# Kernel optimization log

Measured on AMD Instinct MI355X. Metric: run time of the kernel, lower is better.

## Reference

```python
import jax, jax.numpy as jnp
import numpy as np

N = 50000      # nodes
E = 800000     # edges (before self loops)
IN = 256       # in_channels
HID = 64       # hidden_channels
HEADS = 2
NEG_SLOPE = 0.2
BN_EPS = 1e-5


def setup_inputs() -> dict:
    key = jax.random.key(0)
    ks = jax.random.split(key, 16)
    def g(i, shape, scale=0.05):
        return jax.random.normal(ks[i], shape, dtype=jnp.float32) * scale
    return {
        "x": jax.random.normal(ks[0], (N, IN), dtype=jnp.float32),
        "edge_index": jax.random.randint(ks[1], (2, E), 0, N, dtype=jnp.int64).astype(jnp.int32),
        # conv1 (GATv2, heads=2, concat)
        "W1l": g(2, (IN, HEADS * HID)), "b1l": jnp.zeros(HEADS * HID, jnp.float32),
        "W1r": g(3, (IN, HEADS * HID)), "b1r": jnp.zeros(HEADS * HID, jnp.float32),
        "att1": g(4, (HEADS, HID)), "bias1": jnp.zeros(HEADS * HID, jnp.float32),
        "bn1_g": jnp.ones(HEADS * HID, jnp.float32), "bn1_b": jnp.zeros(HEADS * HID, jnp.float32),
        "bn1_m": jnp.zeros(HEADS * HID, jnp.float32), "bn1_v": jnp.ones(HEADS * HID, jnp.float32),
        # conv2 (GATv2, heads=1)
        "W2l": g(5, (HEADS * HID, HID)), "b2l": jnp.zeros(HID, jnp.float32),
        "W2r": g(6, (HEADS * HID, HID)), "b2r": jnp.zeros(HID, jnp.float32),
        "att2": g(7, (1, HID)), "bias2": jnp.zeros(HID, jnp.float32),
        "bn2_g": jnp.ones(HID, jnp.float32), "bn2_b": jnp.zeros(HID, jnp.float32),
        "bn2_m": jnp.zeros(HID, jnp.float32), "bn2_v": jnp.ones(HID, jnp.float32),
        # classifier
        "Wc": g(8, (HID, 1)), "bc": jnp.zeros(1, jnp.float32),
    }


def _gatv2(x, src, dst, Wl, bl, Wr, br, att, bias, heads, ch, n):
    # GATv2: e_ij = att . leaky_relu(Wl x_j + Wr x_i); segment softmax over dst; out_i = sum alpha_ij Wl x_j
    xl = (x @ Wl + bl).reshape(n, heads, ch)  # source transform [N,H,C]
    xr = (x @ Wr + br).reshape(n, heads, ch)  # target transform [N,H,C]
    e = jax.nn.leaky_relu(xl[src] + xr[dst], NEG_SLOPE)        # [E,H,C]
    logits = jnp.einsum('ehc,hc->eh', e, att)                  # [E,H]
    m = jax.ops.segment_max(logits, dst, num_segments=n)       # [N,H]
    p = jnp.exp(logits - m[dst])
    s = jax.ops.segment_sum(p, dst, num_segments=n)            # [N,H]
    alpha = p / s[dst]                                         # [E,H]
    out = jax.ops.segment_sum(alpha[:, :, None] * xl[src], dst, num_segments=n)  # [N,H,C]
    return out.reshape(n, heads * ch) + bias


def _bn(x, g, b, m, v):
    return (x - m) * jax.lax.rsqrt(v + BN_EPS) * g + b


def reference(x, edge_index, W1l, b1l, W1r, b1r, att1, bias1,
              bn1_g, bn1_b, bn1_m, bn1_v,
              W2l, b2l, W2r, b2r, att2, bias2,
              bn2_g, bn2_b, bn2_m, bn2_v, Wc, bc):
    n = x.shape[0]
    loop = jnp.arange(n, dtype=edge_index.dtype)  # add_self_loops=True
    src = jnp.concatenate([edge_index[0], loop])
    dst = jnp.concatenate([edge_index[1], loop])
    h = _gatv2(x, src, dst, W1l, b1l, W1r, b1r, att1, bias1, HEADS, HID, n)
    h = jax.nn.elu(_bn(h, bn1_g, bn1_b, bn1_m, bn1_v))
    h = _gatv2(h, src, dst, W2l, b2l, W2r, b2r, att2, bias2, 1, HID, n)
    h = jax.nn.elu(_bn(h, bn2_g, bn2_b, bn2_m, bn2_v))
    return jax.nn.sigmoid(h @ Wc + bc)
```

## Files before the change

### kernel.cpp

```cpp
#include <hip/hip_runtime.h>
#include <hip/hip_bf16.h>
#include <cstddef>

#define NN 50000
#define EE 800000
#define TE 850000
#define INC 256
#define C1 128
#define C2 64
#define NCHUNK 49

#define NB_COUNT 3321
#define NB_CAST  12500
#define NB_P1    256
#define NB_P2    128
#define NB_K1    (NB_COUNT + NB_CAST + NB_P1 + NB_P2)
#define NB_GEMM1 782
#define NB_K2    (NB_GEMM1 + NB_COUNT)

typedef unsigned short ushort_t;
typedef short bf16x8 __attribute__((ext_vector_type(8)));
typedef float f32x4 __attribute__((ext_vector_type(4)));

__device__ inline ushort_t bf16r(float f) {
    unsigned u = __float_as_uint(f);
    unsigned r = (u + 0x7fffu + ((u >> 16) & 1u)) >> 16;
    return (ushort_t)r;
}
#define LOF(u) (__uint_as_float((u) << 16))
#define HIF(u) (__uint_as_float((u) & 0xffff0000u))
#define LRELU(t) (fmaxf((t), 0.f) + 0.2f * fminf((t), 0.f))
#define ELU(t) ((t) > 0.f ? (t) : (__expf(t) - 1.f))


__global__ void k_scan1(const int* __restrict__ deg, int* __restrict__ incl,
                        int* __restrict__ totals) {
    __shared__ int lds[1024];
    int t = threadIdx.x;
    int i = blockIdx.x * 1024 + t;
    int v = (i < NN) ? deg[i] : 0;
    lds[t] = v;
    __syncthreads();
    for (int off = 1; off < 1024; off <<= 1) {
        int add = (t >= off) ? lds[t - off] : 0;
        __syncthreads();
        lds[t] += add;
        __syncthreads();
    }
    if (i < NN) incl[i] = lds[t];
    if (t == 1023) totals[blockIdx.x] = lds[t];
}

__global__ void k_scan2(const int* __restrict__ totals, int* __restrict__ chunkoff) {
    int t = threadIdx.x;
    int orig = (t < NCHUNK) ? totals[t] : 0;
    int v = orig;
    for (int off = 1; off < 64; off <<= 1) {
        int u = __shfl_up(v, off, 64);
        if (t >= off) v += u;
    }
    if (t < NCHUNK) chunkoff[t] = v - orig;
}

__global__ void k_scan3(const int* __restrict__ incl, const int* __restrict__ deg,
                        const int* __restrict__ chunkoff, int* __restrict__ rowstart) {
    int i = blockIdx.x * blockDim.x + threadIdx.x;
    if (i == 0) rowstart[NN] = TE;
    if (i >= NN) return;
    rowstart[i] = incl[i] - deg[i] + chunkoff[i >> 10];
}


__global__ __launch_bounds__(256) void k_stage1(
    const int* __restrict__ ei, int* __restrict__ deg, int* __restrict__ rank,
    const float* __restrict__ x, ushort_t* __restrict__ xb,
    const float* __restrict__ W1l, const float* __restrict__ W1r,
    const float* __restrict__ b1l, const float* __restrict__ b1r,
    ushort_t* __restrict__ Wt1, float* __restrict__ biasf1,
    const float* __restrict__ W2l, const float* __restrict__ W2r,
    const float* __restrict__ b2l, const float* __restrict__ b2r,
    ushort_t* __restrict__ Wt2, float* __restrict__ biasf2) {
    int b = blockIdx.x;
    int tid = threadIdx.x;
    if (b < NB_COUNT) {
        int e = b * 256 + tid;
        if (e < TE) {
            int dst = (e < EE) ? ei[EE + e] : (e - EE);
            rank[e] = atomicAdd(&deg[dst], 1);
        }
    } else if (b < NB_COUNT + NB_CAST) {
        int i = (b - NB_COUNT) * 256 + tid;
        float4 a = ((const float4*)x)[i];
        ushort4 o;
        o.x = bf16r(a.x); o.y = bf16r(a.y); o.z = bf16r(a.z); o.w = bf16r(a.w);
        ((ushort4*)xb)[i] = o;
    } else if (b < NB_COUNT + NB_CAST + NB_P1) {
        int n = b - NB_COUNT - NB_CAST;
        int k = tid;
        const float* W = (n < 128) ? W1l : W1r;
        int c = (n < 128) ? n : n - 128;
        Wt1[(size_t)n * 256 + k] = bf16r(W[(size_t)k * 128 + c]);
        if (n == 0) biasf1[k] = (k < 128) ? b1l[k] : b1r[k - 128];
    } else {
        int n = b - NB_COUNT - NB_CAST - NB_P1;
        int k = tid;
        if (k < 128) {
            const float* W = (n < 64) ? W2l : W2r;
            int c = (n < 64) ? n : n - 64;
            Wt2[(size_t)n * 128 + k] = bf16r(W[(size_t)k * 64 + c]);
            if (n == 0) biasf2[k] = (k < 64) ? b2l[k] : b2r[k - 64];
        }
    }
}


template <int K, int NCOL>
__device__ inline void gemm_body(const ushort_t* __restrict__ A,
                                 const ushort_t* __restrict__ Bt,
                                 const float* __restrict__ bias,
                                 ushort_t* __restrict__ C, int M,
                                 int bm, int bn, ushort_t* As, ushort_t* Bs) {
    int tid = threadIdx.x;
    int w = tid >> 6, l = tid & 63;
    int wm = (w & 1) * 64, wn = (w >> 1) * 64;
    int lm = l & 15, half = l >> 4;

    f32x4 zero = {0.f, 0.f, 0.f, 0.f};
    f32x4 acc[4][4];
#pragma unroll
    for (int a = 0; a < 4; a++)
#pragma unroll
        for (int b = 0; b < 4; b++) acc[a][b] = zero;

    for (int k0 = 0; k0 < K; k0 += 32) {
#pragma unroll
        for (int q = 0; q < 2; q++) {
            int seg = q * 256 + tid;
            int m = seg >> 2;
            int ko = (seg & 3) * 8;
            *(float4*)&As[m * 40 + ko] = *(const float4*)&A[(size_t)(bm + m) * K + k0 + ko];
            *(float4*)&Bs[m * 40 + ko] = *(const float4*)&Bt[(size_t)(bn + m) * K + k0 + ko];
        }
        __syncthreads();
        bf16x8 af[4], bfr[4];
#pragma unroll
        for (int mi = 0; mi < 4; mi++)
            af[mi] = *(const bf16x8*)&As[(wm + mi * 16 + lm) * 40 + half * 8];
#pragma unroll
        for (int ni = 0; ni < 4; ni++)
            bfr[ni] = *(const bf16x8*)&Bs[(wn + ni * 16 + lm) * 40 + half * 8];
#pragma unroll
        for (int mi = 0; mi < 4; mi++)
#pragma unroll
            for (int ni = 0; ni < 4; ni++)
                acc[mi][ni] = __builtin_amdgcn_mfma_f32_16x16x32_bf16(
                    af[mi], bfr[ni], acc[mi][ni], 0, 0, 0);
        __syncthreads();
    }
#pragma unroll
    for (int ni = 0; ni < 4; ni++) {
        int col = bn + wn + ni * 16 + lm;
        float bv = bias[col];
#pragma unroll
        for (int mi = 0; mi < 4; mi++) {
            int rbase = bm + wm + mi * 16 + half * 4;
#pragma unroll
            for (int r = 0; r < 4; r++) {
                int row = rbase + r;
                if (row < M) C[(size_t)row * NCOL + col] = bf16r(acc[mi][ni][r] + bv);
            }
        }
    }
}


__global__ __launch_bounds__(256) void k_gemm1_scatter(
    const ushort_t* __restrict__ A, const ushort_t* __restrict__ Bt,
    const float* __restrict__ bias, ushort_t* __restrict__ C,
    const int* __restrict__ ei, const int* __restrict__ rank,
    const int* __restrict__ rowstart, int* __restrict__ ssrc) {
    __shared__ __align__(16) ushort_t As[128 * 40];
    __shared__ __align__(16) ushort_t Bs[128 * 40];
    int b = blockIdx.x;
    if (b < NB_GEMM1) {
        int bm = (b >> 1) * 128;
        int bn = (b & 1) * 128;
        gemm_body<256, 256>(A, Bt, bias, C, NN, bm, bn, As, Bs);
    } else {
        int e = (b - NB_GEMM1) * 256 + threadIdx.x;
        if (e < TE) {
            int s, d;
            if (e < EE) { s = ei[e]; d = ei[EE + e]; }
            else        { s = e - EE; d = s; }
            ssrc[rowstart[d] + rank[e]] = s;
        }
    }
}

__global__ __launch_bounds__(256) void k_gemm2(
    const ushort_t* __restrict__ A, const ushort_t* __restrict__ Bt,
    const float* __restrict__ bias, ushort_t* __restrict__ C) {
    __shared__ __align__(16) ushort_t As[128 * 40];
    __shared__ __align__(16) ushort_t Bs[128 * 40];
    int bm = blockIdx.x * 128;
    gemm_body<128, 128>(A, Bt, bias, C, NN, bm, 0, As, Bs);
}


__global__ __launch_bounds__(256) void k_fused1(
    const ushort_t* __restrict__ xlr, const int* __restrict__ rowstart,
    const int* __restrict__ ssrc, const float* __restrict__ att,
    const float* __restrict__ bias,
    const float* __restrict__ g, const float* __restrict__ b,
    const float* __restrict__ m, const float* __restrict__ v,
    ushort_t* __restrict__ out) {
    int lane = threadIdx.x & 63;
    int i = blockIdx.x * 4 + (threadIdx.x >> 6);
    if (i >= NN) return;
    int hw = lane >> 5;
    int c2 = lane & 31;
    uint2 xru = *(const uint2*)&xlr[(size_t)i * 256 + 128 + 4 * c2];
    float xr0 = LOF(xru.x), xr1 = HIF(xru.x), xr2 = LOF(xru.y), xr3 = HIF(xru.y);
    float4 at = *(const float4*)&att[4 * c2];
    int row = rowstart[i], end = rowstart[i + 1];
    float a0 = 0.f, a1 = 0.f, a2 = 0.f, a3 = 0.f, s = 0.f;
    int j = row;
    for (; j + 8 <= end; j += 8) {
        int src[4];
        uint2 u[4];
#pragma unroll
        for (int k = 0; k < 4; k++) src[k] = ssrc[j + 2 * k + hw];
#pragma unroll
        for (int k = 0; k < 4; k++)
            u[k] = *(const uint2*)&xlr[(size_t)src[k] * 256 + 4 * c2];
        float d[4], f0[4], f1[4], f2[4], f3[4];
#pragma unroll
        for (int k = 0; k < 4; k++) {
            f0[k] = LOF(u[k].x); f1[k] = HIF(u[k].x);
            f2[k] = LOF(u[k].y); f3[k] = HIF(u[k].y);
            float t0 = f0[k] + xr0, t1 = f1[k] + xr1;
            float t2 = f2[k] + xr2, t3 = f3[k] + xr3;
            d[k] = at.x * LRELU(t0) + at.y * LRELU(t1)
                 + at.z * LRELU(t2) + at.w * LRELU(t3);
        }
#pragma unroll
        for (int o = 1; o <= 8; o <<= 1) {
#pragma unroll
            for (int k = 0; k < 4; k++) d[k] += __shfl_xor(d[k], o, 64);
        }
#pragma unroll
        for (int k = 0; k < 4; k++) {
            float p = __expf(d[k]);
            a0 += p * f0[k]; a1 += p * f1[k];
            a2 += p * f2[k]; a3 += p * f3[k];
            s += p;
        }
    }
    for (; j < end; j += 2) {
        int je = j + hw;
        bool valid = je < end;
        int src = valid ? ssrc[je] : i;
        uint2 uu = *(const uint2*)&xlr[(size_t)src * 256 + 4 * c2];
        float f0 = LOF(uu.x), f1 = HIF(uu.x), f2 = LOF(uu.y), f3 = HIF(uu.y);
        float t0 = f0 + xr0, t1 = f1 + xr1, t2 = f2 + xr2, t3 = f3 + xr3;
        float d = at.x * LRELU(t0) + at.y * LRELU(t1)
                + at.z * LRELU(t2) + at.w * LRELU(t3);
        d += __shfl_xor(d, 1, 64);
        d += __shfl_xor(d, 2, 64);
        d += __shfl_xor(d, 4, 64);
        d += __shfl_xor(d, 8, 64);
        float p = valid ? __expf(d) : 0.f;
        a0 += p * f0; a1 += p * f1; a2 += p * f2; a3 += p * f3;
        s += p;
    }
    a0 += __shfl_xor(a0, 32, 64);
    a1 += __shfl_xor(a1, 32, 64);
    a2 += __shfl_xor(a2, 32, 64);
    a3 += __shfl_xor(a3, 32, 64);
    s  += __shfl_xor(s, 32, 64);
    if (hw == 0) {
        float inv = 1.f / s;
        float4 bb = *(const float4*)&bias[4 * c2];
        float4 mm = *(const float4*)&m[4 * c2];
        float4 vv = *(const float4*)&v[4 * c2];
        float4 gg = *(const float4*)&g[4 * c2];
        float4 b2 = *(const float4*)&b[4 * c2];
        float o0 = a0 * inv + bb.x, o1 = a1 * inv + bb.y;
        float o2 = a2 * inv + bb.z, o3 = a3 * inv + bb.w;
        o0 = (o0 - mm.x) * rsqrtf(vv.x + 1e-5f) * gg.x + b2.x;
        o1 = (o1 - mm.y) * rsqrtf(vv.y + 1e-5f) * gg.y + b2.y;
        o2 = (o2 - mm.z) * rsqrtf(vv.z + 1e-5f) * gg.z + b2.z;
        o3 = (o3 - mm.w) * rsqrtf(vv.w + 1e-5f) * gg.w + b2.w;
        o0 = ELU(o0); o1 = ELU(o1); o2 = ELU(o2); o3 = ELU(o3);
        uint2 wp;
        wp.x = (unsigned)bf16r(o0) | ((unsigned)bf16r(o1) << 16);
        wp.y = (unsigned)bf16r(o2) | ((unsigned)bf16r(o3) << 16);
        *(uint2*)&out[(size_t)i * C1 + 4 * c2] = wp;
    }
}

__global__ __launch_bounds__(256) void k_fused2(
    const ushort_t* __restrict__ xlr, const int* __restrict__ rowstart,
    const int* __restrict__ ssrc, const float* __restrict__ att,
    const float* __restrict__ bias,
    const float* __restrict__ g, const float* __restrict__ b,
    const float* __restrict__ m, const float* __restrict__ v,
    const float* __restrict__ Wc, const float* __restrict__ bc,
    float* __restrict__ out) {
    int lane = threadIdx.x & 63;
    int i = blockIdx.x * 4 + (threadIdx.x >> 6);
    if (i >= NN) return;
    int qw = lane >> 4;
    int c4 = lane & 15;
    uint2 xru = *(const uint2*)&xlr[(size_t)i * 128 + 64 + 4 * c4];
    float xr0 = LOF(xru.x), xr1 = HIF(xru.x), xr2 = LOF(xru.y), xr3 = HIF(xru.y);
    float4 at = *(const float4*)&att[4 * c4];
    int row = rowstart[i], end = rowstart[i + 1];
    float a0 = 0.f, a1 = 0.f, a2 = 0.f, a3 = 0.f, s = 0.f;
    int j = row;
    for (; j + 8 <= end; j += 8) {
        int src[2];
        uint2 u[2];
#pragma unroll
        for (int k = 0; k < 2; k++) src[k] = ssrc[j + 4 * k + qw];
#pragma unroll
        for (int k = 0; k < 2; k++)
            u[k] = *(const uint2*)&xlr[(size_t)src[k] * 128 + 4 * c4];
        float d[2], f0[2], f1[2], f2[2], f3[2];
#pragma unroll
        for (int k = 0; k < 2; k++) {
            f0[k] = LOF(u[k].x); f1[k] = HIF(u[k].x);
            f2[k] = LOF(u[k].y); f3[k] = HIF(u[k].y);
            float t0 = f0[k] + xr0, t1 = f1[k] + xr1;
            float t2 = f2[k] + xr2, t3 = f3[k] + xr3;
            d[k] = at.x * LRELU(t0) + at.y * LRELU(t1)
                 + at.z * LRELU(t2) + at.w * LRELU(t3);
        }
#pragma unroll
        for (int o = 1; o <= 8; o <<= 1) {
#pragma unroll
            for (int k = 0; k < 2; k++) d[k] += __shfl_xor(d[k], o, 64);
        }
#pragma unroll
        for (int k = 0; k < 2; k++) {
            float p = __expf(d[k]);
            a0 += p * f0[k]; a1 += p * f1[k];
            a2 += p * f2[k]; a3 += p * f3[k];
            s += p;
        }
    }
    for (; j < end; j += 4) {
        int je = j + qw;
        bool valid = je < end;
        int src = valid ? ssrc[je] : i;
        uint2 uu = *(const uint2*)&xlr[(size_t)src * 128 + 4 * c4];
        float f0 = LOF(uu.x), f1 = HIF(uu.x), f2 = LOF(uu.y), f3 = HIF(uu.y);
        float t0 = f0 + xr0, t1 = f1 + xr1, t2 = f2 + xr2, t3 = f3 + xr3;
        float d = at.x * LRELU(t0) + at.y * LRELU(t1)
                + at.z * LRELU(t2) + at.w * LRELU(t3);
        d += __shfl_xor(d, 1, 64);
        d += __shfl_xor(d, 2, 64);
        d += __shfl_xor(d, 4, 64);
        d += __shfl_xor(d, 8, 64);
        float p = valid ? __expf(d) : 0.f;
        a0 += p * f0; a1 += p * f1; a2 += p * f2; a3 += p * f3;
        s += p;
    }
#pragma unroll
    for (int o = 16; o <= 32; o <<= 1) {
        a0 += __shfl_xor(a0, o, 64);
        a1 += __shfl_xor(a1, o, 64);
        a2 += __shfl_xor(a2, o, 64);
        a3 += __shfl_xor(a3, o, 64);
        s  += __shfl_xor(s, o, 64);
    }
    float inv = 1.f / s;
    float4 bb = *(const float4*)&bias[4 * c4];
    float4 mm = *(const float4*)&m[4 * c4];
    float4 vv = *(const float4*)&v[4 * c4];
    float4 gg = *(const float4*)&g[4 * c4];
    float4 b2 = *(const float4*)&b[4 * c4];
    float o0 = a0 * inv + bb.x, o1 = a1 * inv + bb.y;
    float o2 = a2 * inv + bb.z, o3 = a3 * inv + bb.w;
    o0 = (o0 - mm.x) * rsqrtf(vv.x + 1e-5f) * gg.x + b2.x;
    o1 = (o1 - mm.y) * rsqrtf(vv.y + 1e-5f) * gg.y + b2.y;
    o2 = (o2 - mm.z) * rsqrtf(vv.z + 1e-5f) * gg.z + b2.z;
    o3 = (o3 - mm.w) * rsqrtf(vv.w + 1e-5f) * gg.w + b2.w;
    o0 = ELU(o0); o1 = ELU(o1); o2 = ELU(o2); o3 = ELU(o3);
    float4 wc = *(const float4*)&Wc[4 * c4];
    float z = o0 * wc.x + o1 * wc.y + o2 * wc.z + o3 * wc.w;
    z += __shfl_xor(z, 1, 64);
    z += __shfl_xor(z, 2, 64);
    z += __shfl_xor(z, 4, 64);
    z += __shfl_xor(z, 8, 64);
    if (lane == 0) out[i] = 1.f / (1.f + __expf(-(z + bc[0])));
}


extern "C" void kernel_launch(void* const* d_in, const int* in_sizes, int n_in,
                              void* d_out, int out_size, void* d_ws, size_t ws_size,
                              hipStream_t stream) {
    const float* x    = (const float*)d_in[0];
    const int*   ei   = (const int*)d_in[1];
    const float* W1l  = (const float*)d_in[2];
    const float* b1l  = (const float*)d_in[3];
    const float* W1r  = (const float*)d_in[4];
    const float* b1r  = (const float*)d_in[5];
    const float* att1 = (const float*)d_in[6];
    const float* bias1= (const float*)d_in[7];
    const float* bn1g = (const float*)d_in[8];
    const float* bn1b = (const float*)d_in[9];
    const float* bn1m = (const float*)d_in[10];
    const float* bn1v = (const float*)d_in[11];
    const float* W2l  = (const float*)d_in[12];
    const float* b2l  = (const float*)d_in[13];
    const float* W2r  = (const float*)d_in[14];
    const float* b2r  = (const float*)d_in[15];
    const float* att2 = (const float*)d_in[16];
    const float* bias2= (const float*)d_in[17];
    const float* bn2g = (const float*)d_in[18];
    const float* bn2b = (const float*)d_in[19];
    const float* bn2m = (const float*)d_in[20];
    const float* bn2v = (const float*)d_in[21];
    const float* Wc   = (const float*)d_in[22];
    const float* bc   = (const float*)d_in[23];
    float* out = (float*)d_out;

    char* ws = (char*)d_ws;
    size_t off = 0;
    auto alloc = [&](size_t bytes) {
        size_t o = off;
        off += (bytes + 255) & ~(size_t)255;
        return o;
    };
    ushort_t* xb    = (ushort_t*)(ws + alloc((size_t)(NN + 128) * 256 * 2));
    ushort_t* xlr1  = (ushort_t*)(ws + alloc((size_t)NN * 256 * 2));
    ushort_t* h1b   = (ushort_t*)(ws + alloc((size_t)(NN + 128) * 128 * 2));
    ushort_t* Wt1   = (ushort_t*)(ws + alloc((size_t)256 * 256 * 2));
    float*    biasf1= (float*)(ws + alloc(256 * 4));
    ushort_t* Wt2   = (ushort_t*)(ws + alloc((size_t)128 * 128 * 2));
    float*    biasf2= (float*)(ws + alloc(128 * 4));
    int* deg      = (int*)(ws + alloc((size_t)NN * 4));
    int* incl     = (int*)(ws + alloc((size_t)NN * 4));
    int* rowstart = (int*)(ws + alloc((size_t)(NN + 1) * 4));
    int* totals   = (int*)(ws + alloc(64 * 4));
    int* chunkoff = (int*)(ws + alloc(64 * 4));
    int* rank     = (int*)(ws + alloc((size_t)TE * 4));
    int* ssrc     = (int*)(ws + alloc((size_t)TE * 4));
    ushort_t* xlr2 = xlr1;

    hipMemsetAsync(deg, 0, (size_t)NN * 4, stream);

    k_stage1<<<NB_K1, 256, 0, stream>>>(ei, deg, rank, x, xb,
                                        W1l, W1r, b1l, b1r, Wt1, biasf1,
                                        W2l, W2r, b2l, b2r, Wt2, biasf2);

    k_scan1<<<NCHUNK, 1024, 0, stream>>>(deg, incl, totals);
    k_scan2<<<1, 64, 0, stream>>>(totals, chunkoff);
    k_scan3<<<(NN + 255) / 256, 256, 0, stream>>>(incl, deg, chunkoff, rowstart);

    k_gemm1_scatter<<<NB_K2, 256, 0, stream>>>(xb, Wt1, biasf1, xlr1,
                                               ei, rank, rowstart, ssrc);

    k_fused1<<<(NN + 3) / 4, 256, 0, stream>>>(xlr1, rowstart, ssrc, att1, bias1,
                                               bn1g, bn1b, bn1m, bn1v, h1b);

    k_gemm2<<<(NN + 127) / 128, 256, 0, stream>>>(h1b, Wt2, biasf2, xlr2);
    k_fused2<<<(NN + 3) / 4, 256, 0, stream>>>(xlr2, rowstart, ssrc, att2, bias2,
                                               bn2g, bn2b, bn2m, bn2v, Wc, bc, out);
}
```

Before: 307.2 us.

## Widen gather loads to 16B, simplify leaky-relu math, drop scan2 kernel

Both aggregation kernels now have each lane gather 8 bf16 channels (uint4) instead of 4, so more edges are processed in parallel per wave and fewer shuffle reduction steps are needed. Leaky-ReLU is rewritten as 0.6*t+0.4*|t| with log2e folded into the attention weights so exp2f can be used. The separate chunk-offset scan kernel is removed and each thread instead sums the chunk totals in a loop, saving one launch. The scatter blocks are also moved ahead of the GEMM blocks in the combined launch. The trade-offs are more per-thread registers and redundant prefix summation in scan3.

```diff
diff --git a/kernel.cpp b/kernel.cpp
--- a/kernel.cpp
+++ b/kernel.cpp
@@ -16,7 +16,9 @@
 #define NB_P2    128
 #define NB_K1    (NB_COUNT + NB_CAST + NB_P1 + NB_P2)
 #define NB_GEMM1 782
-#define NB_K2    (NB_GEMM1 + NB_COUNT)
+#define NB_K2    (NB_COUNT + NB_GEMM1)
+
+#define LOG2E 1.44269504088896340736f
 
 typedef unsigned short ushort_t;
 typedef short bf16x8 __attribute__((ext_vector_type(8)));
@@ -29,8 +31,12 @@
 }
 #define LOF(u) (__uint_as_float((u) << 16))
 #define HIF(u) (__uint_as_float((u) & 0xffff0000u))
-#define LRELU(t) (fmaxf((t), 0.f) + 0.2f * fminf((t), 0.f))
 #define ELU(t) ((t) > 0.f ? (t) : (__expf(t) - 1.f))
+
+__device__ inline void unpack8(uint4 u, float* f) {
+    f[0] = LOF(u.x); f[1] = HIF(u.x); f[2] = LOF(u.y); f[3] = HIF(u.y);
+    f[4] = LOF(u.z); f[5] = HIF(u.z); f[6] = LOF(u.w); f[7] = HIF(u.w);
+}
 
 
 __global__ void k_scan1(const int* __restrict__ deg, int* __restrict__ incl,
@@ -51,23 +57,15 @@
     if (t == 1023) totals[blockIdx.x] = lds[t];
 }
 
-__global__ void k_scan2(const int* __restrict__ totals, int* __restrict__ chunkoff) {
-    int t = threadIdx.x;
-    int orig = (t < NCHUNK) ? totals[t] : 0;
-    int v = orig;
-    for (int off = 1; off < 64; off <<= 1) {
-        int u = __shfl_up(v, off, 64);
-        if (t >= off) v += u;
-    }
-    if (t < NCHUNK) chunkoff[t] = v - orig;
-}
-
 __global__ void k_scan3(const int* __restrict__ incl, const int* __restrict__ deg,
-                        const int* __restrict__ chunkoff, int* __restrict__ rowstart) {
+                        const int* __restrict__ totals, int* __restrict__ rowstart) {
     int i = blockIdx.x * blockDim.x + threadIdx.x;
     if (i == 0) rowstart[NN] = TE;
     if (i >= NN) return;
-    rowstart[i] = incl[i] - deg[i] + chunkoff[i >> 10];
+    int chunk = blockIdx.x >> 2;
+    int coff = 0;
+    for (int c = 0; c < chunk; c++) coff += totals[c];
+    rowstart[i] = incl[i] - deg[i] + coff;
 }
 
 
@@ -182,18 +180,19 @@
     __shared__ __align__(16) ushort_t As[128 * 40];
     __shared__ __align__(16) ushort_t Bs[128 * 40];
     int b = blockIdx.x;
-    if (b < NB_GEMM1) {
-        int bm = (b >> 1) * 128;
-        int bn = (b & 1) * 128;
-        gemm_body<256, 256>(A, Bt, bias, C, NN, bm, bn, As, Bs);
-    } else {
-        int e = (b - NB_GEMM1) * 256 + threadIdx.x;
+    if (b < NB_COUNT) {
+        int e = b * 256 + threadIdx.x;
         if (e < TE) {
             int s, d;
             if (e < EE) { s = ei[e]; d = ei[EE + e]; }
             else        { s = e - EE; d = s; }
             ssrc[rowstart[d] + rank[e]] = s;
         }
+    } else {
+        int g = b - NB_COUNT;
+        int bm = (g >> 1) * 128;
+        int bn = (g & 1) * 128;
+        gemm_body<256, 256>(A, Bt, bias, C, NN, bm, bn, As, Bs);
     }
 }
 
@@ -217,85 +216,101 @@
     int lane = threadIdx.x & 63;
     int i = blockIdx.x * 4 + (threadIdx.x >> 6);
     if (i >= NN) return;
-    int hw = lane >> 5;
-    int c2 = lane & 31;
-    uint2 xru = *(const uint2*)&xlr[(size_t)i * 256 + 128 + 4 * c2];
-    float xr0 = LOF(xru.x), xr1 = HIF(xru.x), xr2 = LOF(xru.y), xr3 = HIF(xru.y);
-    float4 at = *(const float4*)&att[4 * c2];
+    int es = lane >> 4;
+    int c1 = lane & 15;
+    uint4 xru = *(const uint4*)&xlr[(size_t)i * 256 + 128 + 8 * c1];
+    float xr[8];
+    unpack8(xru, xr);
+    float a6[8], a4[8];
+    {
+        float4 ta = *(const float4*)&att[8 * c1];
+        float4 tb = *(const float4*)&att[8 * c1 + 4];
+        float atv[8] = {ta.x, ta.y, ta.z, ta.w, tb.x, tb.y, tb.z, tb.w};
+#pragma unroll
+        for (int c = 0; c < 8; c++) {
+            a6[c] = atv[c] * (0.6f * LOG2E);
+            a4[c] = atv[c] * (0.4f * LOG2E);
+        }
+    }
     int row = rowstart[i], end = rowstart[i + 1];
-    float a0 = 0.f, a1 = 0.f, a2 = 0.f, a3 = 0.f, s = 0.f;
+    float acc[8] = {};
+    float s = 0.f;
     int j = row;
     for (; j + 8 <= end; j += 8) {
-        int src[4];
-        uint2 u[4];
-#pragma unroll
-        for (int k = 0; k < 4; k++) src[k] = ssrc[j + 2 * k + hw];
-#pragma unroll
-        for (int k = 0; k < 4; k++)
-            u[k] = *(const uint2*)&xlr[(size_t)src[k] * 256 + 4 * c2];
-        float d[4], f0[4], f1[4], f2[4], f3[4];
-#pragma unroll
-        for (int k = 0; k < 4; k++) {
-            f0[k] = LOF(u[k].x); f1[k] = HIF(u[k].x);
-            f2[k] = LOF(u[k].y); f3[k] = HIF(u[k].y);
-            float t0 = f0[k] + xr0, t1 = f1[k] + xr1;
-            float t2 = f2[k] + xr2, t3 = f3[k] + xr3;
-            d[k] = at.x * LRELU(t0) + at.y * LRELU(t1)
-                 + at.z * LRELU(t2) + at.w * LRELU(t3);
-        }
-#pragma unroll
-        for (int o = 1; o <= 8; o <<= 1) {
-#pragma unroll
-            for (int k = 0; k < 4; k++) d[k] += __shfl_xor(d[k], o, 64);
-        }
-#pragma unroll
-        for (int k = 0; k < 4; k++) {
-            float p = __expf(d[k]);
-            a0 += p * f0[k]; a1 += p * f1[k];
-            a2 += p * f2[k]; a3 += p * f3[k];
-            s += p;
-        }
-    }
-    for (; j < end; j += 2) {
-        int je = j + hw;
+        int s0 = ssrc[j + es], s1 = ssrc[j + 4 + es];
+        uint4 u0 = *(const uint4*)&xlr[(size_t)s0 * 256 + 8 * c1];
+        uint4 u1 = *(const uint4*)&xlr[(size_t)s1 * 256 + 8 * c1];
+        float f0[8], f1[8];
+        unpack8(u0, f0);
+        unpack8(u1, f1);
+        float d0 = 0.f, d1 = 0.f;
+#pragma unroll
+        for (int c = 0; c < 8; c++) {
+            float t0 = f0[c] + xr[c];
+            float t1 = f1[c] + xr[c];
+            d0 = fmaf(a6[c], t0, fmaf(a4[c], fabsf(t0), d0));
+            d1 = fmaf(a6[c], t1, fmaf(a4[c], fabsf(t1), d1));
+        }
+        d0 += __shfl_xor(d0, 1, 64); d1 += __shfl_xor(d1, 1, 64);
+        d0 += __shfl_xor(d0, 2, 64); d1 += __shfl_xor(d1, 2, 64);
+        d0 += __shfl_xor(d0, 4, 64); d1 += __shfl_xor(d1, 4, 64);
+        float p0 = exp2f(d0), p1 = exp2f(d1);
+#pragma unroll
+        for (int c = 0; c < 8; c++) acc[c] = fmaf(p0, f0[c], fmaf(p1, f1[c], acc[c]));
+        s += p0 + p1;
+    }
+    for (; j < end; j += 4) {
+        int je = j + es;
         bool valid = je < end;
         int src = valid ? ssrc[je] : i;
-        uint2 uu = *(const uint2*)&xlr[(size_t)src * 256 + 4 * c2];
-        float f0 = LOF(uu.x), f1 = HIF(uu.x), f2 = LOF(uu.y), f3 = HIF(uu.y);
-        float t0 = f0 + xr0, t1 = f1 + xr1, t2 = f2 + xr2, t3 = f3 + xr3;
-        float d = at.x * LRELU(t0) + at.y * LRELU(t1)
-                + at.z * LRELU(t2) + at.w * LRELU(t3);
+        uint4 uu = *(const uint4*)&xlr[(size_t)src * 256 + 8 * c1];
+        float f[8];
+        unpack8(uu, f);
+        float d = 0.f;
+#pragma unroll
+        for (int c = 0; c < 8; c++) {
+            float t = f[c] + xr[c];
+            d = fmaf(a6[c], t, fmaf(a4[c], fabsf(t), d));
+        }
         d += __shfl_xor(d, 1, 64);
         d += __shfl_xor(d, 2, 64);
         d += __shfl_xor(d, 4, 64);
-        d += __shfl_xor(d, 8, 64);
-        float p = valid ? __expf(d) : 0.f;
-        a0 += p * f0; a1 += p * f1; a2 += p * f2; a3 += p * f3;
+        float p = valid ? exp2f(d) : 0.f;
+#pragma unroll
+        for (int c = 0; c < 8; c++) acc[c] = fmaf(p, f[c], acc[c]);
         s += p;
     }
-    a0 += __shfl_xor(a0, 32, 64);
-    a1 += __shfl_xor(a1, 32, 64);
-    a2 += __shfl_xor(a2, 32, 64);
-    a3 += __shfl_xor(a3, 32, 64);
-    s  += __shfl_xor(s, 32, 64);
-    if (hw == 0) {
+#pragma unroll
+    for (int c = 0; c < 8; c++) {
+        acc[c] += __shfl_xor(acc[c], 16, 64);
+        acc[c] += __shfl_xor(acc[c], 32, 64);
+    }
+    s += __shfl_xor(s, 16, 64);
+    s += __shfl_xor(s, 32, 64);
+    if (es == 0) {
         float inv = 1.f / s;
-        float4 bb = *(const float4*)&bias[4 * c2];
-        float4 mm = *(const float4*)&m[4 * c2];
-        float4 vv = *(const float4*)&v[4 * c2];
-        float4 gg = *(const float4*)&g[4 * c2];
-        float4 b2 = *(const float4*)&b[4 * c2];
-        float o0 = a0 * inv + bb.x, o1 = a1 * inv + bb.y;
-        float o2 = a2 * inv + bb.z, o3 = a3 * inv + bb.w;
-        o0 = (o0 - mm.x) * rsqrtf(vv.x + 1e-5f) * gg.x + b2.x;
-        o1 = (o1 - mm.y) * rsqrtf(vv.y + 1e-5f) * gg.y + b2.y;
-        o2 = (o2 - mm.z) * rsqrtf(vv.z + 1e-5f) * gg.z + b2.z;
-        o3 = (o3 - mm.w) * rsqrtf(vv.w + 1e-5f) * gg.w + b2.w;
-        o0 = ELU(o0); o1 = ELU(o1); o2 = ELU(o2); o3 = ELU(o3);
-        uint2 wp;
-        wp.x = (unsigned)bf16r(o0) | ((unsigned)bf16r(o1) << 16);
-        wp.y = (unsigned)bf16r(o2) | ((unsigned)bf16r(o3) << 16);
-        *(uint2*)&out[(size_t)i * C1 + 4 * c2] = wp;
+        float4 bb0 = *(const float4*)&bias[8 * c1], bb1 = *(const float4*)&bias[8 * c1 + 4];
+        float4 mm0 = *(const float4*)&m[8 * c1],   mm1 = *(const float4*)&m[8 * c1 + 4];
+        float4 vv0 = *(const float4*)&v[8 * c1],   vv1 = *(const float4*)&v[8 * c1 + 4];
+        float4 gg0 = *(const float4*)&g[8 * c1],   gg1 = *(const float4*)&g[8 * c1 + 4];
+        float4 be0 = *(const float4*)&b[8 * c1],   be1 = *(const float4*)&b[8 * c1 + 4];
+        float bbv[8] = {bb0.x, bb0.y, bb0.z, bb0.w, bb1.x, bb1.y, bb1.z, bb1.w};
+        float mmv[8] = {mm0.x, mm0.y, mm0.z, mm0.w, mm1.x, mm1.y, mm1.z, mm1.w};
+        float vvv[8] = {vv0.x, vv0.y, vv0.z, vv0.w, vv1.x, vv1.y, vv1.z, vv1.w};
+        float ggv[8] = {gg0.x, gg0.y, gg0.z, gg0.w, gg1.x, gg1.y, gg1.z, gg1.w};
+        float bev[8] = {be0.x, be0.y, be0.z, be0.w, be1.x, be1.y, be1.z, be1.w};
+        unsigned wp[4];
+#pragma unroll
+        for (int c = 0; c < 8; c += 2) {
+            float o0 = acc[c] * inv + bbv[c];
+            float o1 = acc[c + 1] * inv + bbv[c + 1];
+            o0 = (o0 - mmv[c]) * rsqrtf(vvv[c] + 1e-5f) * ggv[c] + bev[c];
+            o1 = (o1 - mmv[c + 1]) * rsqrtf(vvv[c + 1] + 1e-5f) * ggv[c + 1] + bev[c + 1];
+            o0 = ELU(o0); o1 = ELU(o1);
+            wp[c >> 1] = (unsigned)bf16r(o0) | ((unsigned)bf16r(o1) << 16);
+        }
+        uint4 w4 = make_uint4(wp[0], wp[1], wp[2], wp[3]);
+        *(uint4*)&out[(size_t)i * C1 + 8 * c1] = w4;
     }
 }
 
@@ -310,90 +325,106 @@
     int lane = threadIdx.x & 63;
     int i = blockIdx.x * 4 + (threadIdx.x >> 6);
     if (i >= NN) return;
-    int qw = lane >> 4;
-    int c4 = lane & 15;
-    uint2 xru = *(const uint2*)&xlr[(size_t)i * 128 + 64 + 4 * c4];
-    float xr0 = LOF(xru.x), xr1 = HIF(xru.x), xr2 = LOF(xru.y), xr3 = HIF(xru.y);
-    float4 at = *(const float4*)&att[4 * c4];
+    int es = lane >> 3;
+    int cc = lane & 7;
+    uint4 xru = *(const uint4*)&xlr[(size_t)i * 128 + 64 + 8 * cc];
+    float xr[8];
+    unpack8(xru, xr);
+    float a6[8], a4[8];
+    {
+        float4 ta = *(const float4*)&att[8 * cc];
+        float4 tb = *(const float4*)&att[8 * cc + 4];
+        float atv[8] = {ta.x, ta.y, ta.z, ta.w, tb.x, tb.y, tb.z, tb.w};
+#pragma unroll
+        for (int c = 0; c < 8; c++) {
+            a6[c] = atv[c] * (0.6f * LOG2E);
+            a4[c] = atv[c] * (0.4f * LOG2E);
+        }
+    }
     int row = rowstart[i], end = rowstart[i + 1];
-    float a0 = 0.f, a1 = 0.f, a2 = 0.f, a3 = 0.f, s = 0.f;
+    float acc[8] = {};
+    float s = 0.f;
     int j = row;
-    for (; j + 8 <= end; j += 8) {
-        int src[2];
-        uint2 u[2];
-#pragma unroll
-        for (int k = 0; k < 2; k++) src[k] = ssrc[j + 4 * k + qw];
-#pragma unroll
-        for (int k = 0; k < 2; k++)
-            u[k] = *(const uint2*)&xlr[(size_t)src[k] * 128 + 4 * c4];
-        float d[2], f0[2], f1[2], f2[2], f3[2];
-#pragma unroll
-        for (int k = 0; k < 2; k++) {
-            f0[k] = LOF(u[k].x); f1[k] = HIF(u[k].x);
-            f2[k] = LOF(u[k].y); f3[k] = HIF(u[k].y);
-            float t0 = f0[k] + xr0, t1 = f1[k] + xr1;
-            float t2 = f2[k] + xr2, t3 = f3[k] + xr3;
-            d[k] = at.x * LRELU(t0) + at.y * LRELU(t1)
-                 + at.z * LRELU(t2) + at.w * LRELU(t3);
-        }
-#pragma unroll
-        for (int o = 1; o <= 8; o <<= 1) {
-#pragma unroll
-            for (int k = 0; k < 2; k++) d[k] += __shfl_xor(d[k], o, 64);
-        }
-#pragma unroll
-        for (int k = 0; k < 2; k++) {
-            float p = __expf(d[k]);
-            a0 += p * f0[k]; a1 += p * f1[k];
-            a2 += p * f2[k]; a3 += p * f3[k];
-            s += p;
-        }
-    }
-    for (; j < end; j += 4) {
-        int je = j + qw;
+    for (; j + 16 <= end; j += 16) {
+        int s0 = ssrc[j + es], s1 = ssrc[j + 8 + es];
+        uint4 u0 = *(const uint4*)&xlr[(size_t)s0 * 128 + 8 * cc];
+        uint4 u1 = *(const uint4*)&xlr[(size_t)s1 * 128 + 8 * cc];
+        float f0[8], f1[8];
+        unpack8(u0, f0);
+        unpack8(u1, f1);
+        float d0 = 0.f, d1 = 0.f;
+#pragma unroll
+        for (int c = 0; c < 8; c++) {
+            float t0 = f0[c] + xr[c];
+            float t1 = f1[c] + xr[c];
+            d0 = fmaf(a6[c], t0, fmaf(a4[c], fabsf(t0), d0));
+            d1 = fmaf(a6[c], t1, fmaf(a4[c], fabsf(t1), d1));
+        }
+        d0 += __shfl_xor(d0, 1, 64); d1 += __shfl_xor(d1, 1, 64);
+        d0 += __shfl_xor(d0, 2, 64); d1 += __shfl_xor(d1, 2, 64);
+        d0 += __shfl_xor(d0, 4, 64); d1 += __shfl_xor(d1, 4, 64);
+        float p0 = exp2f(d0), p1 = exp2f(d1);
+#pragma unroll
+        for (int c = 0; c < 8; c++) acc[c] = fmaf(p0, f0[c], fmaf(p1, f1[c], acc[c]));
+        s += p0 + p1;
+    }
+    for (; j < end; j += 8) {
+        int je = j + es;
         bool valid = je < end;
         int src = valid ? ssrc[je] : i;
-        uint2 uu = *(const uint2*)&xlr[(size_t)src * 128 + 4 * c4];
-        float f0 = LOF(uu.x), f1 = HIF(uu.x), f2 = LOF(uu.y), f3 = HIF(uu.y);
-        float t0 = f0 + xr0, t1 = f1 + xr1, t2 = f2 + xr2, t3 = f3 + xr3;
-        float d = at.x * LRELU(t0) + at.y * LRELU(t1)
-                + at.z * LRELU(t2) + at.w * LRELU(t3);
+        uint4 uu = *(const uint4*)&xlr[(size_t)src * 128 + 8 * cc];
+        float f[8];
+        unpack8(uu, f);
+        float d = 0.f;
+#pragma unroll
+        for (int c = 0; c < 8; c++) {
+            float t = f[c] + xr[c];
+            d = fmaf(a6[c], t, fmaf(a4[c], fabsf(t), d));
+        }
         d += __shfl_xor(d, 1, 64);
         d += __shfl_xor(d, 2, 64);
         d += __shfl_xor(d, 4, 64);
-        d += __shfl_xor(d, 8, 64);
-        float p = valid ? __expf(d) : 0.f;
-        a0 += p * f0; a1 += p * f1; a2 += p * f2; a3 += p * f3;
+        float p = valid ? exp2f(d) : 0.f;
+#pragma unroll
+        for (int c = 0; c < 8; c++) acc[c] = fmaf(p, f[c], acc[c]);
         s += p;
     }
 #pragma unroll
-    for (int o = 16; o <= 32; o <<= 1) {
-        a0 += __shfl_xor(a0, o, 64);
-        a1 += __shfl_xor(a1, o, 64);
-        a2 += __shfl_xor(a2, o, 64);
-        a3 += __shfl_xor(a3, o, 64);
-        s  += __shfl_xor(s, o, 64);
-    }
-    float inv = 1.f / s;
-    float4 bb = *(const float4*)&bias[4 * c4];
-    float4 mm = *(const float4*)&m[4 * c4];
-    float4 vv = *(const float4*)&v[4 * c4];
-    float4 gg = *(const float4*)&g[4 * c4];
-    float4 b2 = *(const float4*)&b[4 * c4];
-    float o0 = a0 * inv + bb.x, o1 = a1 * inv + bb.y;
-    float o2 = a2 * inv + bb.z, o3 = a3 * inv + bb.w;
-    o0 = (o0 - mm.x) * rsqrtf(vv.x + 1e-5f) * gg.x + b2.x;
-    o1 = (o1 - mm.y) * rsqrtf(vv.y + 1e-5f) * gg.y + b2.y;
-    o2 = (o2 - mm.z) * rsqrtf(vv.z + 1e-5f) * gg.z + b2.z;
-    o3 = (o3 - mm.w) * rsqrtf(vv.w + 1e-5f) * gg.w + b2.w;
-    o0 = ELU(o0); o1 = ELU(o1); o2 = ELU(o2); o3 = ELU(o3);
-    float4 wc = *(const float4*)&Wc[4 * c4];
-    float z = o0 * wc.x + o1 * wc.y + o2 * wc.z + o3 * wc.w;
-    z += __shfl_xor(z, 1, 64);
-    z += __shfl_xor(z, 2, 64);
-    z += __shfl_xor(z, 4, 64);
-    z += __shfl_xor(z, 8, 64);
-    if (lane == 0) out[i] = 1.f / (1.f + __expf(-(z + bc[0])));
+    for (int c = 0; c < 8; c++) {
+        acc[c] += __shfl_xor(acc[c], 8, 64);
+        acc[c] += __shfl_xor(acc[c], 16, 64);
+        acc[c] += __shfl_xor(acc[c], 32, 64);
+    }
+    s += __shfl_xor(s, 8, 64);
+    s += __shfl_xor(s, 16, 64);
+    s += __shfl_xor(s, 32, 64);
+    if (es == 0) {
+        float inv = 1.f / s;
+        float4 bb0 = *(const float4*)&bias[8 * cc], bb1 = *(const float4*)&bias[8 * cc + 4];
+        float4 mm0 = *(const float4*)&m[8 * cc],   mm1 = *(const float4*)&m[8 * cc + 4];
+        float4 vv0 = *(const float4*)&v[8 * cc],   vv1 = *(const float4*)&v[8 * cc + 4];
+        float4 gg0 = *(const float4*)&g[8 * cc],   gg1 = *(const float4*)&g[8 * cc + 4];
+        float4 be0 = *(const float4*)&b[8 * cc],   be1 = *(const float4*)&b[8 * cc + 4];
+        float4 wc0 = *(const float4*)&Wc[8 * cc],  wc1 = *(const float4*)&Wc[8 * cc + 4];
+        float bbv[8] = {bb0.x, bb0.y, bb0.z, bb0.w, bb1.x, bb1.y, bb1.z, bb1.w};
+        float mmv[8] = {mm0.x, mm0.y, mm0.z, mm0.w, mm1.x, mm1.y, mm1.z, mm1.w};
+        float vvv[8] = {vv0.x, vv0.y, vv0.z, vv0.w, vv1.x, vv1.y, vv1.z, vv1.w};
+        float ggv[8] = {gg0.x, gg0.y, gg0.z, gg0.w, gg1.x, gg1.y, gg1.z, gg1.w};
+        float bev[8] = {be0.x, be0.y, be0.z, be0.w, be1.x, be1.y, be1.z, be1.w};
+        float wcv[8] = {wc0.x, wc0.y, wc0.z, wc0.w, wc1.x, wc1.y, wc1.z, wc1.w};
+        float z = 0.f;
+#pragma unroll
+        for (int c = 0; c < 8; c++) {
+            float o = acc[c] * inv + bbv[c];
+            o = (o - mmv[c]) * rsqrtf(vvv[c] + 1e-5f) * ggv[c] + bev[c];
+            o = ELU(o);
+            z = fmaf(o, wcv[c], z);
+        }
+        z += __shfl_xor(z, 1, 64);
+        z += __shfl_xor(z, 2, 64);
+        z += __shfl_xor(z, 4, 64);
+        if (cc == 0) out[i] = 1.f / (1.f + __expf(-(z + bc[0])));
+    }
 }
 
 
@@ -444,7 +475,6 @@
     int* incl     = (int*)(ws + alloc((size_t)NN * 4));
     int* rowstart = (int*)(ws + alloc((size_t)(NN + 1) * 4));
     int* totals   = (int*)(ws + alloc(64 * 4));
-    int* chunkoff = (int*)(ws + alloc(64 * 4));
     int* rank     = (int*)(ws + alloc((size_t)TE * 4));
     int* ssrc     = (int*)(ws + alloc((size_t)TE * 4));
     ushort_t* xlr2 = xlr1;
@@ -456,8 +486,7 @@
                                         W2l, W2r, b2l, b2r, Wt2, biasf2);
 
     k_scan1<<<NCHUNK, 1024, 0, stream>>>(deg, incl, totals);
-    k_scan2<<<1, 64, 0, stream>>>(totals, chunkoff);
-    k_scan3<<<(NN + 255) / 256, 256, 0, stream>>>(incl, deg, chunkoff, rowstart);
+    k_scan3<<<(NN + 255) / 256, 256, 0, stream>>>(incl, deg, totals, rowstart);
 
     k_gemm1_scatter<<<NB_K2, 256, 0, stream>>>(xb, Wt1, biasf1, xlr1,
                                                ei, rank, rowstart, ssrc);
```

New measurement: 321.6 us. 1.05x slower.
